# Performance work log

Hardware: AMD Instinct MI355X
Metric: run time of the kernel (lower is better)

## Reference

```python
import jax, jax.numpy as jnp
from jax import lax
import numpy as np

B, S, W = 32, 256, 16
WORD_VOCAB, WORD_DIM = 100000, 300
CHAR_VOCAB, CHAR_DIM = 101, 16  # len(char_vocab)+1
CH, WH = 16, 32                 # char_lstm_dim, lstm_size
GEN = 100
N_LABELS = 2


def _lstm(x, Wih, Whh, b, reverse=False):
    """Single-direction LSTM. x: [T, N, D]. Returns (outputs [T,N,H], final h [N,H]).
    Torch gate order: i, f, g, o."""
    pre = jnp.einsum('tnd,hd->tnh', x, Wih) + b  # [T, N, 4H]
    if reverse:
        pre = pre[::-1]
    H = Whh.shape[1]
    N = x.shape[1]

    def step(carry, xt):
        h, c = carry
        g = xt + h @ Whh.T
        i, f, gg, o = jnp.split(g, 4, axis=-1)
        c = jax.nn.sigmoid(f) * c + jax.nn.sigmoid(i) * jnp.tanh(gg)
        h = jax.nn.sigmoid(o) * jnp.tanh(c)
        return (h, c), h

    init = (jnp.zeros((N, H), x.dtype), jnp.zeros((N, H), x.dtype))
    (hT, _), hs = lax.scan(step, init, pre)
    if reverse:
        hs = hs[::-1]
    return hs, hT


def setup_inputs() -> dict:
    key = jax.random.key(0)
    ks = jax.random.split(key, 16)
    sc = lambda *shape: 0.1

    def rn(k, shape):
        return jax.random.normal(k, shape, dtype=jnp.float32) * 0.1

    return {
        'word_ids': jax.random.randint(ks[0], (B, S), 0, WORD_VOCAB),
        'char_ids': jax.random.randint(ks[1], (B, S, W), 0, CHAR_VOCAB),
        'word_table': rn(ks[2], (WORD_VOCAB, WORD_DIM)),
        'char_table': rn(ks[3], (CHAR_VOCAB, CHAR_DIM)),
        'c_Wih_f': rn(ks[4], (4 * CH, CHAR_DIM)), 'c_Whh_f': rn(ks[5], (4 * CH, CH)),
        'c_b_f': jnp.zeros((4 * CH,), jnp.float32),
        'c_Wih_b': rn(ks[6], (4 * CH, CHAR_DIM)), 'c_Whh_b': rn(ks[7], (4 * CH, CH)),
        'c_b_b': jnp.zeros((4 * CH,), jnp.float32),
        'gen_W': rn(ks[8], (GEN, WORD_DIM + 2 * CH)), 'gen_b': jnp.zeros((GEN,), jnp.float32),
        'w_Wih_f': rn(ks[9], (4 * WH, GEN)), 'w_Whh_f': rn(ks[10], (4 * WH, WH)),
        'w_b_f': jnp.zeros((4 * WH,), jnp.float32),
        'w_Wih_b': rn(ks[11], (4 * WH, GEN)), 'w_Whh_b': rn(ks[12], (4 * WH, WH)),
        'w_b_b': jnp.zeros((4 * WH,), jnp.float32),
        'out_W': rn(ks[13], (N_LABELS, 2 * WH)), 'out_b': jnp.zeros((N_LABELS,), jnp.float32),
    }


def reference(word_ids, char_ids, word_table, char_table,
              c_Wih_f, c_Whh_f, c_b_f, c_Wih_b, c_Whh_b, c_b_b,
              gen_W, gen_b,
              w_Wih_f, w_Whh_f, w_b_f, w_Wih_b, w_Whh_b, w_b_b,
              out_W, out_b):
    # Word embedding lookup: [B, S, WORD_DIM]
    word_e = word_table[word_ids]
    # Char embedding: [B, S, W, CHAR_DIM] -> char biLSTM over W, final states.
    char_e = char_table[char_ids].reshape(B * S, W, CHAR_DIM).transpose(1, 0, 2)  # [W, B*S, C]
    _, hf = _lstm(char_e, c_Wih_f, c_Whh_f, c_b_f, reverse=False)
    _, hb = _lstm(char_e, c_Wih_b, c_Whh_b, c_b_b, reverse=True)
    char_repr = jnp.concatenate([hf, hb], axis=-1).reshape(B, S, 2 * CH)
    # Concat word + char reprs, gen layer + gelu (dropout p=0 / eval).
    word_output = jnp.concatenate([word_e, char_repr], axis=-1)  # [B, S, 332]
    word_vecs = jax.nn.gelu(word_output @ gen_W.T + gen_b, approximate=False)  # [B, S, GEN]
    # Word-level biLSTM over S, per-step outputs.
    x = word_vecs.transpose(1, 0, 2)  # [S, B, GEN]
    of, _ = _lstm(x, w_Wih_f, w_Whh_f, w_b_f, reverse=False)
    ob, _ = _lstm(x, w_Wih_b, w_Whh_b, w_b_b, reverse=True)
    lstm_out = jnp.concatenate([of, ob], axis=-1).transpose(1, 0, 2)  # [B, S, 2*WH]
    # Output layer + sigmoid.
    return jax.nn.sigmoid(lstm_out @ out_W.T + out_b)  # [B, S, N_LABELS]
```

## Files before the change

kernel.cpp:

```cpp
#include <hip/hip_runtime.h>
#include <hip/hip_bf16.h>

#define B_    32
#define S_    256
#define BS_   8192
#define Wc_   16
#define CDIM_ 16
#define CH_   16
#define WDIM_ 300
#define KX_   332
#define XC_   336
#define GEN_  100
#define WVP_  104
#define WH_   32
#define NG_   128

constexpr size_t OFF_WV   = 0;
constexpr size_t OFF_PRE  = OFF_WV   + (size_t)BS_*WVP_;
constexpr size_t OFF_LO   = OFF_PRE  + (size_t)2*S_*B_*NG_;
constexpr size_t OFF_CHB  = OFF_LO   + (size_t)BS_*64;
constexpr size_t OFF_GWT  = OFF_CHB  + (size_t)BS_*32;
constexpr size_t OFF_WIHT = OFF_GWT  + (size_t)KX_*128;
constexpr size_t OFF_WHHT = OFF_WIHT + (size_t)2*GEN_*NG_;
constexpr size_t OFF_OW   = OFF_WHHT + (size_t)2*WH_*NG_;

__device__ __forceinline__ float sigm(float x){ return __builtin_amdgcn_rcpf(1.f + __expf(-x)); }
__device__ __forceinline__ float tanh_(float x){ return 1.f - 2.f*__builtin_amdgcn_rcpf(1.f + __expf(2.f*x)); }
__device__ __forceinline__ float rdlane(float v, int lane){
  return __uint_as_float(__builtin_amdgcn_readlane(__float_as_uint(v), lane));
}

__global__ void k_prep(const float* gen_W, const float* wih_f, const float* wih_b,
                       const float* whh_f, const float* whh_b, const float* out_W,
                       float* ws){
  int idx = blockIdx.x*blockDim.x + threadIdx.x;
  int stride = gridDim.x*blockDim.x;
  for (int i = idx; i < GEN_*KX_; i += stride){
    int j = i / KX_, k = i - j*KX_;
    ws[OFF_GWT + (size_t)k*128 + j] = gen_W[i];
  }
  for (int i = idx; i < NG_*GEN_; i += stride){
    int g = i / GEN_, k = i - g*GEN_;
    ws[OFF_WIHT + 0*GEN_*NG_ + (size_t)k*NG_ + g] = wih_f[i];
    ws[OFF_WIHT + 1*GEN_*NG_ + (size_t)k*NG_ + g] = wih_b[i];
  }
  for (int i = idx; i < NG_*WH_; i += stride){
    int g = i / WH_, k = i - g*WH_;
    ws[OFF_WHHT + 0*WH_*NG_ + (size_t)k*NG_ + g] = whh_f[i];
    ws[OFF_WHHT + 1*WH_*NG_ + (size_t)k*NG_ + g] = whh_b[i];
  }
  for (int i = idx; i < 2*64; i += stride) ws[OFF_OW + i] = out_W[i];
}

__global__ void __launch_bounds__(256, 2) k_char(const int* char_ids, const float* char_table,
                       const float* Wih_f, const float* Whh_f, const float* b_f,
                       const float* Wih_b, const float* Whh_b, const float* b_b,
                       float* ws){
  __shared__ float xr[16*324];
  const int dir = blockIdx.x & 1;
  const int sg  = blockIdx.x >> 1;
  const int tid = threadIdx.x;
  const float* WI = dir ? Wih_b : Wih_f;
  const float* WH = dir ? Whh_b : Whh_f;
  const float* BB = dir ? b_b  : b_f;
  const int ls = tid >> 4, u = tid & 15;
  const int seq0 = sg * 16;
  {
    const int id = char_ids[(seq0 + ls)*Wc_ + u];
    const float4* sr = (const float4*)(char_table + (size_t)id*CDIM_);
    float4 v0 = sr[0], v1 = sr[1], v2 = sr[2], v3 = sr[3];
    float* xw = &xr[ls*324 + u*20];
    *(float4*)(xw+0)  = v0; *(float4*)(xw+4)  = v1;
    *(float4*)(xw+8)  = v2; *(float4*)(xw+12) = v3;
  }
  float wi[4][16];
  #pragma unroll
  for (int g = 0; g < 4; ++g){
    const float4* wr = (const float4*)(WI + (size_t)(g*16+u)*CDIM_);
    float4 a = wr[0], b = wr[1], c = wr[2], d = wr[3];
    wi[g][0]=a.x; wi[g][1]=a.y; wi[g][2]=a.z; wi[g][3]=a.w;
    wi[g][4]=b.x; wi[g][5]=b.y; wi[g][6]=b.z; wi[g][7]=b.w;
    wi[g][8]=c.x; wi[g][9]=c.y; wi[g][10]=c.z; wi[g][11]=c.w;
    wi[g][12]=d.x; wi[g][13]=d.y; wi[g][14]=d.z; wi[g][15]=d.w;
  }
  float bias[4];
  #pragma unroll
  for (int g = 0; g < 4; ++g) bias[g] = BB[g*16+u];
  __syncthreads();
  float xp[16][4];
  const float* xb = &xr[ls*324];
  #pragma unroll
  for (int p = 0; p < 16; ++p){
    const int tm = dir ? (15-p) : p;
    const float4 x0 = *(const float4*)(xb + tm*20 + 0);
    const float4 x1 = *(const float4*)(xb + tm*20 + 4);
    const float4 x2 = *(const float4*)(xb + tm*20 + 8);
    const float4 x3 = *(const float4*)(xb + tm*20 + 12);
    float xk[16] = {x0.x,x0.y,x0.z,x0.w, x1.x,x1.y,x1.z,x1.w,
                    x2.x,x2.y,x2.z,x2.w, x3.x,x3.y,x3.z,x3.w};
    #pragma unroll
    for (int g = 0; g < 4; ++g){
      float a0 = bias[g], a1 = 0.f;
      #pragma unroll
      for (int k = 0; k < 16; k += 2){ a0 += wi[g][k]*xk[k]; a1 += wi[g][k+1]*xk[k+1]; }
      xp[p][g] = a0 + a1;
    }
  }
  float wh[4][16];
  #pragma unroll
  for (int g = 0; g < 4; ++g){
    const float4* wr = (const float4*)(WH + (size_t)(g*16+u)*CH_);
    float4 a = wr[0], b = wr[1], c = wr[2], d = wr[3];
    wh[g][0]=a.x; wh[g][1]=a.y; wh[g][2]=a.z; wh[g][3]=a.w;
    wh[g][4]=b.x; wh[g][5]=b.y; wh[g][6]=b.z; wh[g][7]=b.w;
    wh[g][8]=c.x; wh[g][9]=c.y; wh[g][10]=c.z; wh[g][11]=c.w;
    wh[g][12]=d.x; wh[g][13]=d.y; wh[g][14]=d.z; wh[g][15]=d.w;
  }
  const int lbase = (tid & 63) & 48;
  float h = 0.f, c = 0.f;
  #pragma unroll
  for (int p = 0; p < 16; ++p){
    float ai = xp[p][0], af = xp[p][1], ag = xp[p][2], ao = xp[p][3];
    #pragma unroll
    for (int k = 0; k < 16; ++k){
      const float hk = __shfl(h, lbase + k, 64);
      ai += wh[0][k]*hk; af += wh[1][k]*hk;
      ag += wh[2][k]*hk; ao += wh[3][k]*hk;
    }
    c = sigm(af)*c + sigm(ai)*tanh_(ag);
    h = sigm(ao)*tanh_(c);
  }
  ws[OFF_CHB + (size_t)(seq0 + ls)*32 + dir*16 + u] = h;
}

__global__ void k_gen(const int* word_ids, const float* word_table, const float* gen_b, float* ws){
  __shared__ __align__(16) float xt[16*XC_];
  __shared__ int wids[16];
  const int r0 = blockIdx.x*16;
  if (threadIdx.x < 16) wids[threadIdx.x] = word_ids[r0 + threadIdx.x];
  __syncthreads();
  float4* xt4 = (float4*)xt;
  for (int i = threadIdx.x; i < 16*75; i += 128){
    const int r = i/75, q = i - r*75;
    xt4[r*84 + q] = ((const float4*)(word_table + (size_t)wids[r]*WDIM_))[q];
  }
  for (int i = threadIdx.x; i < 16*8; i += 128){
    const int r = i >> 3, q = i & 7;
    xt4[r*84 + 75 + q] = ((const float4*)(ws + OFF_CHB + (size_t)(r0+r)*32))[q];
  }
  __syncthreads();
  const int j = threadIdx.x;
  const float bj = (j < GEN_) ? gen_b[j] : 0.f;
  float acc[16];
  #pragma unroll
  for (int r = 0; r < 16; ++r) acc[r] = bj;
  const float* WT = ws + OFF_GWT;
  for (int k4 = 0; k4 < KX_/4; ++k4){
    const int k = k4*4;
    const float w0 = WT[(size_t)(k+0)*128 + j];
    const float w1 = WT[(size_t)(k+1)*128 + j];
    const float w2 = WT[(size_t)(k+2)*128 + j];
    const float w3 = WT[(size_t)(k+3)*128 + j];
    #pragma unroll
    for (int r = 0; r < 16; ++r){
      const float4 xv = xt4[r*84 + k4];
      acc[r] += w0*xv.x + w1*xv.y + w2*xv.z + w3*xv.w;
    }
  }
  if (j < GEN_){
    float* wv = ws + OFF_WV;
    #pragma unroll
    for (int r = 0; r < 16; ++r){
      const float a = acc[r];
      wv[(size_t)(r0+r)*WVP_ + j] = 0.5f*a*(1.f + erff(a*0.70710678118f));
    }
  }
}

__global__ void k_wpre(const float* wb_f, const float* wb_b, float* ws){
  __shared__ __align__(16) float xt[8*WVP_];
  const int d  = blockIdx.x & 1;
  const int r0 = (blockIdx.x >> 1)*8;
  const float4* WVr = (const float4*)(ws + OFF_WV + (size_t)r0*WVP_);
  float4* xt4 = (float4*)xt;
  for (int i = threadIdx.x; i < 8*(WVP_/4); i += 128) xt4[i] = WVr[i];
  __syncthreads();
  const int g = threadIdx.x;
  const float wb = (d ? wb_b : wb_f)[g];
  float acc[8];
  #pragma unroll
  for (int r = 0; r < 8; ++r) acc[r] = wb;
  const float* WT = ws + OFF_WIHT + (size_t)d*GEN_*NG_;
  for (int k4 = 0; k4 < GEN_/4; ++k4){
    const int k = k4*4;
    const float w0 = WT[(size_t)(k+0)*NG_ + g];
    const float w1 = WT[(size_t)(k+1)*NG_ + g];
    const float w2 = WT[(size_t)(k+2)*NG_ + g];
    const float w3 = WT[(size_t)(k+3)*NG_ + g];
    #pragma unroll
    for (int r = 0; r < 8; ++r){
      const float4 xv = xt4[r*(WVP_/4) + k4];
      acc[r] += w0*xv.x + w1*xv.y + w2*xv.z + w3*xv.w;
    }
  }
  float* pre = ws + OFF_PRE + (size_t)d*S_*B_*NG_;
  #pragma unroll
  for (int r = 0; r < 8; ++r){
    const int row = r0 + r, b = row >> 8, s = row & 255;
    pre[((size_t)s*B_ + b)*NG_ + g] = acc[r];
  }
}

#define HRPAD_ 5632
__global__ void __launch_bounds__(64) k_wlstm(const float* __restrict__ WHT,
                                              const float* __restrict__ PRE,
                                              float* __restrict__ LO){
  __shared__ __align__(16) float hring[HRPAD_];
  const int pair = blockIdx.x;
  const int d = pair >> 5;
  const int n = pair & 31;
  const int l = threadIdx.x;
  const float* WT = WHT + (size_t)d*WH_*NG_;
  float wA[32], wB[32];
  #pragma unroll
  for (int k = 0; k < 32; ++k){ wA[k] = WT[(size_t)k*NG_ + l]; wB[k] = WT[(size_t)k*NG_ + 64 + l]; }
  const float* pre = PRE + (size_t)d*S_*B_*NG_ + (size_t)n*NG_;
  const float* p0 = pre + (size_t)(d ? (S_-1) : 0)*B_*NG_;
  const ptrdiff_t stp = (d ? -1 : 1) * (ptrdiff_t)(B_*NG_);
  float cst = 0.f, h = 0.f;

  float a0A = p0[0*stp + l], a0B = p0[0*stp + 64 + l];
  float a1A = p0[1*stp + l], a1B = p0[1*stp + 64 + l];
  float a2A = p0[2*stp + l], a2B = p0[2*stp + 64 + l];
  float a3A = p0[3*stp + l], a3B = p0[3*stp + 64 + l];

#define WSTEP(pAv, pBv, sidx) { \
    float aA0 = (pAv), aA1 = 0.f, aA2 = 0.f, aA3 = 0.f; \
    float aB0 = (pBv), aB1 = 0.f, aB2 = 0.f, aB3 = 0.f; \
    _Pragma("unroll") \
    for (int k = 0; k < 32; k += 4){ \
      const float h0 = rdlane(h, k+0); \
      const float h1 = rdlane(h, k+1); \
      const float h2 = rdlane(h, k+2); \
      const float h3 = rdlane(h, k+3); \
      aA0 += wA[k+0]*h0; aB0 += wB[k+0]*h0; \
      aA1 += wA[k+1]*h1; aB1 += wB[k+1]*h1; \
      aA2 += wA[k+2]*h2; aB2 += wB[k+2]*h2; \
      aA3 += wA[k+3]*h3; aB3 += wB[k+3]*h3; \
    } \
    const float aA = (aA0+aA1)+(aA2+aA3);    \
    const float aB = (aB0+aB1)+(aB2+aB3);    \
    const float fga = __shfl_xor(aA, 32);    \
    const float oga = __shfl_xor(aB, 32);    \
    const float cc = sigm(fga)*cst + sigm(aA)*tanh_(aB);   \
    cst = cc; \
    h = sigm(oga)*tanh_(cc);                                \
    if (l < 32) hring[((sidx) & 31)*36 + l] = h; \
  }

  for (int t = 0; t < S_; t += 4){
    float n0A=0.f, n0B=0.f, n1A=0.f, n1B=0.f, n2A=0.f, n2B=0.f, n3A=0.f, n3B=0.f;
    if (t + 4 < S_){
      const float* q = p0 + (ptrdiff_t)(t+4)*stp;
      n0A = q[0*stp + l]; n0B = q[0*stp + 64 + l];
      n1A = q[1*stp + l]; n1B = q[1*stp + 64 + l];
      n2A = q[2*stp + l]; n2B = q[2*stp + 64 + l];
      n3A = q[3*stp + l]; n3B = q[3*stp + 64 + l];
    }
    WSTEP(a0A, a0B, t+0)
    WSTEP(a1A, a1B, t+1)
    WSTEP(a2A, a2B, t+2)
    WSTEP(a3A, a3B, t+3)
    a0A=n0A; a0B=n0B; a1A=n1A; a1B=n1B;
    a2A=n2A; a2B=n2B; a3A=n3A; a3B=n3B;

    if ((t & 31) == 28){
      const int s0 = t & ~31;
      const int srow = l >> 1, half = l & 1;
      const int s = s0 + srow;
      const int ss = d ? (S_ - 1 - s) : s;
      const float4* src = (const float4*)&hring[srow*36 + half*16];
      float4* dst = (float4*)(LO + ((size_t)n*S_ + ss)*64 + d*32 + half*16);
      dst[0] = src[0]; dst[1] = src[1]; dst[2] = src[2]; dst[3] = src[3];
    }
  }
#undef WSTEP
}

__global__ void k_out(const float* ws, const float* out_b, float* out){
  const int row = blockIdx.x*blockDim.x + threadIdx.x;
  const float4* lo = (const float4*)(ws + OFF_LO + (size_t)row*64);
  const float* OW = ws + OFF_OW;
  float a0 = out_b[0], a1 = out_b[1];
  #pragma unroll
  for (int q = 0; q < 16; ++q){
    const float4 v = lo[q];
    a0 += OW[q*4+0]*v.x + OW[q*4+1]*v.y + OW[q*4+2]*v.z + OW[q*4+3]*v.w;
    a1 += OW[64+q*4+0]*v.x + OW[64+q*4+1]*v.y + OW[64+q*4+2]*v.z + OW[64+q*4+3]*v.w;
  }
  out[row*2+0] = sigm(a0);
  out[row*2+1] = sigm(a1);
}

extern "C" void kernel_launch(void* const* d_in, const int* in_sizes, int n_in,
                              void* d_out, int out_size, void* d_ws, size_t ws_size,
                              hipStream_t stream){
  (void)in_sizes; (void)n_in; (void)out_size; (void)ws_size;
  const int*   word_ids   = (const int*)  d_in[0];
  const int*   char_ids   = (const int*)  d_in[1];
  const float* word_table = (const float*)d_in[2];
  const float* char_table = (const float*)d_in[3];
  const float* c_Wih_f    = (const float*)d_in[4];
  const float* c_Whh_f    = (const float*)d_in[5];
  const float* c_b_f      = (const float*)d_in[6];
  const float* c_Wih_b    = (const float*)d_in[7];
  const float* c_Whh_b    = (const float*)d_in[8];
  const float* c_b_b      = (const float*)d_in[9];
  const float* gen_W      = (const float*)d_in[10];
  const float* gen_b      = (const float*)d_in[11];
  const float* w_Wih_f    = (const float*)d_in[12];
  const float* w_Whh_f    = (const float*)d_in[13];
  const float* w_b_f      = (const float*)d_in[14];
  const float* w_Wih_b    = (const float*)d_in[15];
  const float* w_Whh_b    = (const float*)d_in[16];
  const float* w_b_b      = (const float*)d_in[17];
  const float* out_W      = (const float*)d_in[18];
  const float* out_b      = (const float*)d_in[19];
  float* ws  = (float*)d_ws;
  float* out = (float*)d_out;

  hipLaunchKernelGGL(k_prep,  dim3(64),   dim3(256), 0, stream,
                     gen_W, w_Wih_f, w_Wih_b, w_Whh_f, w_Whh_b, out_W, ws);
  hipLaunchKernelGGL(k_char,  dim3(1024), dim3(256), 0, stream,
                     char_ids, char_table, c_Wih_f, c_Whh_f, c_b_f,
                     c_Wih_b, c_Whh_b, c_b_b, ws);
  hipLaunchKernelGGL(k_gen,   dim3(512),  dim3(128), 0, stream, word_ids, word_table, gen_b, ws);
  hipLaunchKernelGGL(k_wpre,  dim3(2048), dim3(128), 0, stream, w_b_f, w_b_b, ws);
  hipLaunchKernelGGL(k_wlstm, dim3(64),   dim3(64),  0, stream,
                     ws + OFF_WHHT, ws + OFF_PRE, ws + OFF_LO);
  hipLaunchKernelGGL(k_out,   dim3(64),   dim3(128), 0, stream, ws, out_b, out);
}
```

Before: 191.7 us.

## Fuse gen layer with word LSTM input projection and pack recurrent FMAs

Merges the gen+GELU kernel with the word-LSTM input-projection kernel, so the GELU outputs stay in shared memory rather than being written to and re-read from global memory, and one launch is removed. The recurrent matvec in the word LSTM now uses two-wide float vectors so the compiler can emit packed FMAs on the serial critical path. The sigmoid and tanh helpers call exp2 directly with prescaled arguments. The fused kernel uses fewer blocks for the projection work (512 instead of 2048), which lowers parallelism for that stage.

Result: faster. 187.5 us (-2.2%).

```diff
diff --git a/kernel.cpp b/kernel.cpp
--- a/kernel.cpp
+++ b/kernel.cpp
@@ -24,8 +24,14 @@
 constexpr size_t OFF_WHHT = OFF_WIHT + (size_t)2*GEN_*NG_;
 constexpr size_t OFF_OW   = OFF_WHHT + (size_t)2*WH_*NG_;
 
-__device__ __forceinline__ float sigm(float x){ return __builtin_amdgcn_rcpf(1.f + __expf(-x)); }
-__device__ __forceinline__ float tanh_(float x){ return 1.f - 2.f*__builtin_amdgcn_rcpf(1.f + __expf(2.f*x)); }
+typedef __attribute__((ext_vector_type(2))) float f2;
+
+__device__ __forceinline__ float sigm(float x){
+  return __builtin_amdgcn_rcpf(1.f + __builtin_amdgcn_exp2f(-1.44269504089f*x));
+}
+__device__ __forceinline__ float tanh_(float x){
+  return 1.f - 2.f*__builtin_amdgcn_rcpf(1.f + __builtin_amdgcn_exp2f(2.88539008178f*x));
+}
 __device__ __forceinline__ float rdlane(float v, int lane){
   return __uint_as_float(__builtin_amdgcn_readlane(__float_as_uint(v), lane));
 }
@@ -133,8 +139,10 @@
   ws[OFF_CHB + (size_t)(seq0 + ls)*32 + dir*16 + u] = h;
 }
 
-__global__ void k_gen(const int* word_ids, const float* word_table, const float* gen_b, float* ws){
+__global__ void k_genp(const int* word_ids, const float* word_table, const float* gen_b,
+                       const float* wb_f, const float* wb_b, float* ws){
   __shared__ __align__(16) float xt[16*XC_];
+  __shared__ __align__(16) float wvs[16*WVP_];
   __shared__ int wids[16];
   const int r0 = blockIdx.x*16;
   if (threadIdx.x < 16) wids[threadIdx.x] = word_ids[r0 + threadIdx.x];
@@ -168,65 +176,60 @@
     }
   }
   if (j < GEN_){
-    float* wv = ws + OFF_WV;
     #pragma unroll
     for (int r = 0; r < 16; ++r){
       const float a = acc[r];
-      wv[(size_t)(r0+r)*WVP_ + j] = 0.5f*a*(1.f + erff(a*0.70710678118f));
-    }
-  }
-}
-
-__global__ void k_wpre(const float* wb_f, const float* wb_b, float* ws){
-  __shared__ __align__(16) float xt[8*WVP_];
-  const int d  = blockIdx.x & 1;
-  const int r0 = (blockIdx.x >> 1)*8;
-  const float4* WVr = (const float4*)(ws + OFF_WV + (size_t)r0*WVP_);
-  float4* xt4 = (float4*)xt;
-  for (int i = threadIdx.x; i < 8*(WVP_/4); i += 128) xt4[i] = WVr[i];
+      wvs[r*WVP_ + j] = 0.5f*a*(1.f + erff(a*0.70710678118f));
+    }
+  }
   __syncthreads();
   const int g = threadIdx.x;
-  const float wb = (d ? wb_b : wb_f)[g];
-  float acc[8];
-  #pragma unroll
-  for (int r = 0; r < 8; ++r) acc[r] = wb;
-  const float* WT = ws + OFF_WIHT + (size_t)d*GEN_*NG_;
-  for (int k4 = 0; k4 < GEN_/4; ++k4){
-    const int k = k4*4;
-    const float w0 = WT[(size_t)(k+0)*NG_ + g];
-    const float w1 = WT[(size_t)(k+1)*NG_ + g];
-    const float w2 = WT[(size_t)(k+2)*NG_ + g];
-    const float w3 = WT[(size_t)(k+3)*NG_ + g];
-    #pragma unroll
-    for (int r = 0; r < 8; ++r){
-      const float4 xv = xt4[r*(WVP_/4) + k4];
-      acc[r] += w0*xv.x + w1*xv.y + w2*xv.z + w3*xv.w;
-    }
-  }
-  float* pre = ws + OFF_PRE + (size_t)d*S_*B_*NG_;
-  #pragma unroll
-  for (int r = 0; r < 8; ++r){
-    const int row = r0 + r, b = row >> 8, s = row & 255;
-    pre[((size_t)s*B_ + b)*NG_ + g] = acc[r];
-  }
-}
-
-#define HRPAD_ 5632
+  #pragma unroll
+  for (int d = 0; d < 2; ++d){
+    const float* W2 = ws + OFF_WIHT + (size_t)d*GEN_*NG_;
+    const float wb = (d ? wb_b : wb_f)[g];
+    float ac2[16];
+    #pragma unroll
+    for (int r = 0; r < 16; ++r) ac2[r] = wb;
+    for (int k4 = 0; k4 < GEN_/4; ++k4){
+      const int k = k4*4;
+      const float w0 = W2[(size_t)(k+0)*NG_ + g];
+      const float w1 = W2[(size_t)(k+1)*NG_ + g];
+      const float w2 = W2[(size_t)(k+2)*NG_ + g];
+      const float w3 = W2[(size_t)(k+3)*NG_ + g];
+      #pragma unroll
+      for (int r = 0; r < 16; ++r){
+        const float4 xv = *(const float4*)&wvs[r*WVP_ + k];
+        ac2[r] += w0*xv.x + w1*xv.y + w2*xv.z + w3*xv.w;
+      }
+    }
+    float* pre = ws + OFF_PRE + (size_t)d*S_*B_*NG_;
+    #pragma unroll
+    for (int r = 0; r < 16; ++r){
+      const int row = r0 + r, bb = row >> 8, ss = row & 255;
+      pre[((size_t)ss*B_ + bb)*NG_ + g] = ac2[r];
+    }
+  }
+}
+
+#define BN_ ((size_t)B_*NG_)
 __global__ void __launch_bounds__(64) k_wlstm(const float* __restrict__ WHT,
                                               const float* __restrict__ PRE,
                                               float* __restrict__ LO){
-  __shared__ __align__(16) float hring[HRPAD_];
+  __shared__ __align__(16) float hring[5632];
   const int pair = blockIdx.x;
   const int d = pair >> 5;
   const int n = pair & 31;
   const int l = threadIdx.x;
   const float* WT = WHT + (size_t)d*WH_*NG_;
-  float wA[32], wB[32];
-  #pragma unroll
-  for (int k = 0; k < 32; ++k){ wA[k] = WT[(size_t)k*NG_ + l]; wB[k] = WT[(size_t)k*NG_ + 64 + l]; }
-  const float* pre = PRE + (size_t)d*S_*B_*NG_ + (size_t)n*NG_;
-  const float* p0 = pre + (size_t)(d ? (S_-1) : 0)*B_*NG_;
-  const ptrdiff_t stp = (d ? -1 : 1) * (ptrdiff_t)(B_*NG_);
+  f2 w2[32];
+  #pragma unroll
+  for (int k = 0; k < 32; ++k){
+    w2[k] = (f2){ WT[(size_t)k*NG_ + l], WT[(size_t)k*NG_ + 64 + l] };
+  }
+  const float* pre = PRE + (size_t)d*S_*BN_ + (size_t)n*NG_;
+  const float* p0 = pre + (size_t)(d ? (S_-1) : 0)*BN_;
+  const ptrdiff_t stp = (d ? -1 : 1) * (ptrdiff_t)BN_;
   float cst = 0.f, h = 0.f;
 
   float a0A = p0[0*stp + l], a0B = p0[0*stp + 64 + l];
@@ -235,21 +238,21 @@
   float a3A = p0[3*stp + l], a3B = p0[3*stp + 64 + l];
 
 #define WSTEP(pAv, pBv, sidx) { \
-    float aA0 = (pAv), aA1 = 0.f, aA2 = 0.f, aA3 = 0.f; \
-    float aB0 = (pBv), aB1 = 0.f, aB2 = 0.f, aB3 = 0.f; \
+    f2 q0 = (f2){(pAv),(pBv)}, q1 = (f2){0.f,0.f}, q2 = (f2){0.f,0.f}, q3 = (f2){0.f,0.f}; \
     _Pragma("unroll") \
     for (int k = 0; k < 32; k += 4){ \
       const float h0 = rdlane(h, k+0); \
       const float h1 = rdlane(h, k+1); \
       const float h2 = rdlane(h, k+2); \
       const float h3 = rdlane(h, k+3); \
-      aA0 += wA[k+0]*h0; aB0 += wB[k+0]*h0; \
-      aA1 += wA[k+1]*h1; aB1 += wB[k+1]*h1; \
-      aA2 += wA[k+2]*h2; aB2 += wB[k+2]*h2; \
-      aA3 += wA[k+3]*h3; aB3 += wB[k+3]*h3; \
+      q0 += w2[k+0] * (f2){h0,h0}; \
+      q1 += w2[k+1] * (f2){h1,h1}; \
+      q2 += w2[k+2] * (f2){h2,h2}; \
+      q3 += w2[k+3] * (f2){h3,h3}; \
     } \
-    const float aA = (aA0+aA1)+(aA2+aA3);    \
-    const float aB = (aB0+aB1)+(aB2+aB3);    \
+    const f2 qs = (q0+q1)+(q2+q3); \
+    const float aA = qs.x;                   \
+    const float aB = qs.y;                   \
     const float fga = __shfl_xor(aA, 32);    \
     const float oga = __shfl_xor(aB, 32);    \
     const float cc = sigm(fga)*cst + sigm(aA)*tanh_(aB);   \
@@ -334,8 +337,8 @@
   hipLaunchKernelGGL(k_char,  dim3(1024), dim3(256), 0, stream,
                      char_ids, char_table, c_Wih_f, c_Whh_f, c_b_f,
                      c_Wih_b, c_Whh_b, c_b_b, ws);
-  hipLaunchKernelGGL(k_gen,   dim3(512),  dim3(128), 0, stream, word_ids, word_table, gen_b, ws);
-  hipLaunchKernelGGL(k_wpre,  dim3(2048), dim3(128), 0, stream, w_b_f, w_b_b, ws);
+  hipLaunchKernelGGL(k_genp,  dim3(512),  dim3(128), 0, stream,
+                     word_ids, word_table, gen_b, w_b_f, w_b_b, ws);
   hipLaunchKernelGGL(k_wlstm, dim3(64),   dim3(64),  0, stream,
                      ws + OFF_WHHT, ws + OFF_PRE, ws + OFF_LO);
   hipLaunchKernelGGL(k_out,   dim3(64),   dim3(128), 0, stream, ws, out_b, out);
```
